# Kernel tuning notes

Hardware: AMD Instinct MI355X
Metric: run time of the kernel (lower is better)

The kernel has to match this reference:

```python
import jax, jax.numpy as jnp
import numpy as np

B = 131072
T = 30
H = 150
STATIC_D = 50


def _expm_sym2x2(S):
    """Closed-form V diag(exp(e)) V^T for symmetric (B,2,2) S.

    Equals exp(tr/2) * (cosh(d) I + sinh(d)/d * (S - tr/2 I)), d = sqrt(((a-c)/2)^2 + b^2).
    This is exactly what torch.symeig + exp(e) reconstruction computes.
    """
    a = S[:, 0, 0]
    b = S[:, 0, 1]
    c = S[:, 1, 1]
    half_tr = 0.5 * (a + c)
    half_diff = 0.5 * (a - c)
    disc = jnp.sqrt(half_diff * half_diff + b * b)
    d = jnp.maximum(disc, 1e-12)
    sinhc = jnp.sinh(d) / d
    coshd = jnp.cosh(disc)
    scale = jnp.exp(half_tr)
    m00 = scale * (coshd + sinhc * half_diff)
    m11 = scale * (coshd - sinhc * half_diff)
    m01 = scale * (sinhc * b)
    row0 = jnp.stack([m00, m01], axis=-1)
    row1 = jnp.stack([m01, m11], axis=-1)
    return jnp.stack([row0, row1], axis=-2)  # (B,2,2)


def setup_inputs() -> dict:
    key = jax.random.key(0)
    ks = jax.random.split(key, 12)
    s = lambda fan_in: 1.0 / np.sqrt(fan_in)
    inp = {
        "static": jax.random.normal(ks[0], (B, STATIC_D), jnp.float32),
        "init_velocity": jax.random.normal(ks[1], (B, 2), jnp.float32),
        "init_position": jax.random.normal(ks[2], (B, 2), jnp.float32),
        "z": jax.random.normal(ks[3], (T, B, 2), jnp.float32),
        # GRU params (PyTorch layout: gates [r, z, n] stacked along dim 0)
        "W_ih": jax.random.uniform(ks[4], (3 * H, T * 2), jnp.float32, -s(H), s(H)),
        "W_hh": jax.random.uniform(ks[5], (3 * H, H), jnp.float32, -s(H), s(H)),
        "b_ih": jax.random.uniform(ks[6], (3 * H,), jnp.float32, -s(H), s(H)),
        "b_hh": jax.random.uniform(ks[7], (3 * H,), jnp.float32, -s(H), s(H)),
        # MLP params
        "W1": jax.random.uniform(ks[8], (50, H + STATIC_D), jnp.float32, -s(H + STATIC_D), s(H + STATIC_D)),
        "b1": jax.random.uniform(ks[9], (50,), jnp.float32, -s(H + STATIC_D), s(H + STATIC_D)),
        "W2": jax.random.uniform(ks[10], (6, 50), jnp.float32, -s(50), s(50)),
        "b2": jax.random.uniform(ks[11], (6,), jnp.float32, -s(50), s(50)),
    }
    return inp


def reference(static, init_velocity, init_position, z, W_ih, W_hh, b_ih, b_hh, W1, b1, W2, b2):
    batch = static.shape[0]
    h0 = jnp.zeros((batch, H), jnp.float32)
    xbuf0 = jnp.zeros((batch, T, 2), jnp.float32)

    def step(carry, inp):
        h, xbuf, dx, x_prev = carry
        i, zi = inp
        x_flat = xbuf.reshape(batch, T * 2)
        # GRU cell (single layer, seq_len 1)
        gi = x_flat @ W_ih.T + b_ih
        gh = h @ W_hh.T + b_hh
        ir, iz, inn = jnp.split(gi, 3, axis=1)
        hr, hz, hn = jnp.split(gh, 3, axis=1)
        r = jax.nn.sigmoid(ir + hr)
        zg = jax.nn.sigmoid(iz + hz)
        n = jnp.tanh(inn + r * hn)
        h_new = (1.0 - zg) * n + zg * h
        # MLP on [dynamic_encoding, static]
        ds = jnp.concatenate([h_new, static], axis=1)
        o = jax.nn.softplus(ds @ W1.T + b1)
        o = jax.nn.softplus(o @ W2.T + b2)
        mu_hat = o[:, :2]
        sig_hat = o[:, 2:].reshape(batch, 2, 2)
        S = sig_hat + jnp.swapaxes(sig_hat, 1, 2)
        sigma = _expm_sym2x2(S)
        mu = x_prev + dx + mu_hat
        x_ = jnp.einsum('bij,bj->bi', sigma, zi) + mu
        xbuf = jax.lax.dynamic_update_slice(xbuf, x_[:, None, :], (0, i, 0))
        return (h_new, xbuf, x_ - x_prev, x_), (mu, sigma, x_)

    _, (mu, sigma, x) = jax.lax.scan(
        step, (h0, xbuf0, init_velocity, init_position), (jnp.arange(T), z)
    )
    return mu, sigma, x  # (30,B,2), (30,B,2,2), (30,B,2)
```

## Files before the change

### kernel.cpp

```cpp
#include <hip/hip_runtime.h>
#include <math.h>


typedef _Float16 f16;
typedef _Float16 f16x8 __attribute__((ext_vector_type(8)));
typedef float    f32x4 __attribute__((ext_vector_type(4)));

constexpr int BTOT = 131072;
constexpr int TSTEPS = 30;
constexpr int H  = 150;
constexpr int SD = 50;
constexpr int BT = 16;
constexpr int NT = 512;
constexpr int NBLK = 256;
constexpr int NGRP = BTOT / (NBLK * BT);

constexpr int HP = 160;
constexpr int NP = 480;
constexpr int AHS = 232;
constexpr int O1S = 72;

constexpr int WS_WIHT  = 0;
constexpr int WS_BFRAG = 115200;

constexpr int SIG_OFF = TSTEPS * BTOT * 2;
constexpr int X_OFF   = SIG_OFF + TSTEPS * BTOT * 4;

__device__ __forceinline__ float fexp(float x)  { return __builtin_amdgcn_exp2f(x * 1.44269504f); }
__device__ __forceinline__ float sigm(float x)  { return __builtin_amdgcn_rcpf(1.f + __builtin_amdgcn_exp2f(-1.44269504f * x)); }
__device__ __forceinline__ float tanh_(float x) { return fmaf(-2.f, __builtin_amdgcn_rcpf(1.f + __builtin_amdgcn_exp2f(2.88539008f * x)), 1.f); }
__device__ __forceinline__ float softplus_(float v) {
    float e = __builtin_amdgcn_exp2f(-1.44269504f * fabsf(v));
    return fmaxf(v, 0.f) + 0.69314718f * __builtin_amdgcn_logf(1.f + e);
}

__global__ void r2p2_prep(const float* __restrict__ Wih, float* __restrict__ ws) {
    int id = blockIdx.x * 256 + threadIdx.x;
    if (id >= TSTEPS * NP) return;
    int s = id / NP, tp = id - s * NP;
    int g = tp / HP, off = tp - g * HP;
    float2 v = make_float2(0.f, 0.f);
    if (off < H) {
        const float* row = Wih + (g * H + off) * (2 * TSTEPS);
        v.x = row[2 * s];
        v.y = row[2 * s + 1];
    }
    ((float2*)ws)[id] = v;
}

__global__ void r2p2_prep2(const float* __restrict__ Whh, f16* __restrict__ wsB) {
    int id = blockIdx.x * 256 + threadIdx.x;
    if (id >= 9600) return;
    int lane = id & 63, rest = id >> 6;
    int kk = rest % 5, kg = rest / 5;
    int g = kg % 3, k = kg / 3;
    int lr = lane & 15, lq = lane >> 4;
    int nr = k * 16 + lr;
    f16x8 v;
    #pragma unroll
    for (int j = 0; j < 8; ++j) {
        int cc = kk * 32 + lq * 8 + j;
        float x = (nr < H && cc < H) ? Whh[(g * H + nr) * H + cc] : 0.f;
        v[j] = (f16)x;
    }
    *(f16x8*)(wsB + (size_t)id * 8) = v;
}

__global__ __launch_bounds__(NT, 2) void r2p2_main(
    const float* __restrict__ statp, const float* __restrict__ initv,
    const float* __restrict__ initp, const float* __restrict__ zp,
    const float* __restrict__ bih,   const float* __restrict__ bhh,
    const float* __restrict__ W1,    const float* __restrict__ b1,
    const float* __restrict__ W2,    const float* __restrict__ b2,
    const float* __restrict__ wihT,  const f16* __restrict__ wsB,
    float* __restrict__ out)
{
    __shared__ __align__(16) f16   sA[BT * AHS];
    __shared__ __align__(16) f16   sW1[64 * AHS];
    __shared__ __align__(16) f16   sO1[16 * O1S];
    __shared__ __align__(16) f16   sW2[16 * O1S];
    __shared__ __align__(16) float sO2[16 * 8];
    __shared__ __align__(16) float sZ[TSTEPS * 32];
    __shared__ __align__(16) float sOUT[TSTEPS * 16 * 8];
    __shared__ __align__(16) float sXC[32];
    __shared__ __align__(16) float sXP[32];
    __shared__ __align__(16) float sDX[32];

    const int t  = threadIdx.x;
    const int w  = t >> 6;
    const int l  = t & 63;
    const int lr = l & 15;
    const int lq = l >> 4;

    int ntr = 0, tr0 = 0;
    if (w < 4)       { ntr = 1; tr0 = w; }
    else if (w >= 5) { ntr = 2; tr0 = 4 + (w - 5) * 2; }

    for (int i = t; i < BT * AHS / 2; i += NT) ((unsigned*)sA)[i] = 0u;
    for (int i = t; i < 64 * AHS; i += NT) {
        int r = i / AHS, k = i - r * AHS;
        float v = 0.f;
        if (r < SD && k < 224) {
            if (k < H) v = W1[r * 200 + k];
            else if (k >= HP && k < HP + SD) v = W1[r * 200 + H + (k - HP)];
        }
        sW1[i] = (f16)v;
    }
    for (int i = t; i < 16 * O1S; i += NT) {
        int r = i / O1S, k = i - r * O1S;
        sW2[i] = (f16)((r < 6 && k < SD) ? W2[r * SD + k] : 0.f);
        sO1[i] = (f16)0.f;
    }

    f16x8 bfrag[2][3][5];
    #pragma unroll
    for (int tt = 0; tt < 2; ++tt) {
        if (tt < ntr) {
            int k = tr0 + tt;
            #pragma unroll
            for (int g = 0; g < 3; ++g)
                #pragma unroll
                for (int kk = 0; kk < 5; ++kk)
                    bfrag[tt][g][kk] = *(const f16x8*)(wsB + ((size_t)((k * 3 + g) * 5 + kk) * 64 + l) * 8);
        }
    }
    float cR[2], cZ[2], cNi[2], cNh[2];
    #pragma unroll
    for (int tt = 0; tt < 2; ++tt) {
        cR[tt] = cZ[tt] = cNi[tt] = cNh[tt] = 0.f;
        if (tt < ntr) {
            int u = (tr0 + tt) * 16 + lr;
            if (u < H) {
                cR[tt]  = bih[u]         + bhh[u];
                cZ[tt]  = bih[H + u]     + bhh[H + u];
                cNi[tt] = bih[2 * H + u];
                cNh[tt] = bhh[2 * H + u];
            }
        }
    }
    const int   p3col  = w * 16 + lr;
    const float b1reg  = (w < 4 && p3col < SD) ? b1[p3col] : 0.f;
    const float b2reg  = (lr < 6) ? b2[lr] : 0.f;

    float hreg[2][4];
    f32x4 acc[2][3];
    f32x4 gi[2][3];
    float2 wvp[2][3];

    for (int grp = 0; grp < NGRP; ++grp) {
        const int bg0 = (grp * NBLK + blockIdx.x) * BT;
        __syncthreads();
        for (int i = t; i < BT * SD; i += NT) {
            int b = i / SD, k = i - b * SD;
            sA[b * AHS + HP + k] = (f16)statp[(bg0 + b) * SD + k];
        }
        for (int i = t; i < TSTEPS * 32; i += NT)
            sZ[i] = zp[((size_t)(i >> 5) * BTOT + bg0) * 2 + (i & 31)];
        if (t < 2 * BT) {
            sXP[t] = initp[bg0 * 2 + t];
            sDX[t] = initv[bg0 * 2 + t];
        }
        #pragma unroll
        for (int tt = 0; tt < 2; ++tt) {
            #pragma unroll
            for (int j = 0; j < 4; ++j) hreg[tt][j] = 0.f;
            #pragma unroll
            for (int g = 0; g < 3; ++g) acc[tt][g] = (f32x4){0.f, 0.f, 0.f, 0.f};
            gi[tt][0] = (f32x4){cR[tt],  cR[tt],  cR[tt],  cR[tt]};
            gi[tt][1] = (f32x4){cZ[tt],  cZ[tt],  cZ[tt],  cZ[tt]};
            gi[tt][2] = (f32x4){cNi[tt], cNi[tt], cNi[tt], cNi[tt]};
        }
        __syncthreads();

        for (int s = 0; s < TSTEPS; ++s) {
            if (ntr > 0) {
                if (s > 0) {
                    f32x4 xa = *(const f32x4*)&sXC[lq * 8];
                    f32x4 xb = *(const f32x4*)&sXC[lq * 8 + 4];
                    #pragma unroll
                    for (int tt = 0; tt < 2; ++tt) {
                        if (tt < ntr) {
                            #pragma unroll
                            for (int g = 0; g < 3; ++g) {
                                float2 wv = wvp[tt][g];
                                gi[tt][g][0] = fmaf(wv.x, xa[0], fmaf(wv.y, xa[1], gi[tt][g][0]));
                                gi[tt][g][1] = fmaf(wv.x, xa[2], fmaf(wv.y, xa[3], gi[tt][g][1]));
                                gi[tt][g][2] = fmaf(wv.x, xb[0], fmaf(wv.y, xb[1], gi[tt][g][2]));
                                gi[tt][g][3] = fmaf(wv.x, xb[2], fmaf(wv.y, xb[3], gi[tt][g][3]));
                            }
                        }
                    }
                }
                #pragma unroll
                for (int tt = 0; tt < 2; ++tt) {
                    if (tt < ntr) {
                        int u = (tr0 + tt) * 16 + lr;
                        #pragma unroll
                        for (int j = 0; j < 4; ++j) {
                            float r  = sigm(acc[tt][0][j] + gi[tt][0][j]);
                            float zg = sigm(acc[tt][1][j] + gi[tt][1][j]);
                            float n  = tanh_(gi[tt][2][j] + r * (acc[tt][2][j] + cNh[tt]));
                            float hv = (1.f - zg) * n + zg * hreg[tt][j];
                            hreg[tt][j] = hv;
                            if (u < H) sA[(lq * 4 + j) * AHS + u] = (f16)hv;
                        }
                    }
                }
            }
            __syncthreads();

            if (ntr > 0 && s + 1 < TSTEPS) {
                const float* wT = wihT + (size_t)s * (NP * 2);
                #pragma unroll
                for (int tt = 0; tt < 2; ++tt) {
                    if (tt < ntr) {
                        int u = (tr0 + tt) * 16 + lr;
                        #pragma unroll
                        for (int g = 0; g < 3; ++g)
                            wvp[tt][g] = *(const float2*)(wT + (g * HP + u) * 2);
                    }
                }
            }

            if (w < 4) {
                f32x4 a3 = (f32x4){0.f, 0.f, 0.f, 0.f};
                #pragma unroll
                for (int kk = 0; kk < 7; ++kk) {
                    f16x8 av = *(const f16x8*)(sA  + lr    * AHS + kk * 32 + lq * 8);
                    f16x8 bv = *(const f16x8*)(sW1 + p3col * AHS + kk * 32 + lq * 8);
                    a3 = __builtin_amdgcn_mfma_f32_16x16x32_f16(av, bv, a3, 0, 0, 0);
                }
                if (p3col < SD) {
                    #pragma unroll
                    for (int j = 0; j < 4; ++j)
                        sO1[(lq * 4 + j) * O1S + p3col] = (f16)softplus_(a3[j] + b1reg);
                }
            } else if (w >= 5 && s + 1 < TSTEPS) {
                f16x8 af[5];
                #pragma unroll
                for (int kk = 0; kk < 5; ++kk)
                    af[kk] = *(const f16x8*)(sA + lr * AHS + kk * 32 + lq * 8);
                #pragma unroll
                for (int tt = 0; tt < 2; ++tt) {
                    #pragma unroll
                    for (int g = 0; g < 3; ++g) {
                        acc[tt][g] = (f32x4){0.f, 0.f, 0.f, 0.f};
                        #pragma unroll
                        for (int kk = 0; kk < 5; ++kk)
                            acc[tt][g] = __builtin_amdgcn_mfma_f32_16x16x32_f16(af[kk], bfrag[tt][g][kk], acc[tt][g], 0, 0, 0);
                    }
                }
            }
            __syncthreads();

            if (w == 4) {
                f32x4 a4 = (f32x4){0.f, 0.f, 0.f, 0.f};
                #pragma unroll
                for (int kk = 0; kk < 2; ++kk) {
                    f16x8 av = *(const f16x8*)(sO1 + lr * O1S + kk * 32 + lq * 8);
                    f16x8 bv = *(const f16x8*)(sW2 + lr * O1S + kk * 32 + lq * 8);
                    a4 = __builtin_amdgcn_mfma_f32_16x16x32_f16(av, bv, a4, 0, 0, 0);
                }
                if (lr < 6) {
                    #pragma unroll
                    for (int j = 0; j < 4; ++j)
                        sO2[(lq * 4 + j) * 8 + lr] = softplus_(a4[j] + b2reg);
                }
                asm volatile("s_waitcnt lgkmcnt(0)" ::: "memory");
                if (l < BT) {
                    const int b = l;
                    f32x4  v0 = *(const f32x4*)&sO2[b * 8];
                    float2 v1 = *(const float2*)&sO2[b * 8 + 4];
                    float mh0 = v0[0], mh1 = v0[1];
                    float a = 2.f * v0[2], bb2 = v0[3] + v1.x, c = 2.f * v1.y;
                    float htr = 0.5f * (a + c), hdf = 0.5f * (a - c);
                    float disc = sqrtf(hdf * hdf + bb2 * bb2);
                    float d = fmaxf(disc, 1e-12f);
                    float ep = fexp(d), em = fexp(-d);
                    float sinhc = (0.5f * (ep - em)) * __builtin_amdgcn_rcpf(d);
                    float coshd = 0.5f * (ep + em);
                    float scale = fexp(htr);
                    float m00 = scale * (coshd + sinhc * hdf);
                    float m11 = scale * (coshd - sinhc * hdf);
                    float m01 = scale * (sinhc * bb2);

                    float z0 = sZ[s * 32 + 2 * b], z1 = sZ[s * 32 + 2 * b + 1];
                    float xp0 = sXP[2 * b], xp1 = sXP[2 * b + 1];
                    float mu0 = xp0 + sDX[2 * b]     + mh0;
                    float mu1 = xp1 + sDX[2 * b + 1] + mh1;
                    float x0 = fmaf(m00, z0, fmaf(m01, z1, mu0));
                    float x1 = fmaf(m01, z0, fmaf(m11, z1, mu1));

                    float* st = &sOUT[(s * 16 + b) * 8];
                    *(float4*)(st)     = make_float4(mu0, mu1, m00, m01);
                    *(float4*)(st + 4) = make_float4(m11, x0, x1, 0.f);

                    sXC[2 * b] = x0;       sXC[2 * b + 1] = x1;
                    sDX[2 * b] = x0 - xp0; sDX[2 * b + 1] = x1 - xp1;
                    sXP[2 * b] = x0;       sXP[2 * b + 1] = x1;
                }
            } else if (w < 4 && s + 1 < TSTEPS) {
                f16x8 af[5];
                #pragma unroll
                for (int kk = 0; kk < 5; ++kk)
                    af[kk] = *(const f16x8*)(sA + lr * AHS + kk * 32 + lq * 8);
                #pragma unroll
                for (int g = 0; g < 3; ++g) {
                    acc[0][g] = (f32x4){0.f, 0.f, 0.f, 0.f};
                    #pragma unroll
                    for (int kk = 0; kk < 5; ++kk)
                        acc[0][g] = __builtin_amdgcn_mfma_f32_16x16x32_f16(af[kk], bfrag[0][g][kk], acc[0][g], 0, 0, 0);
                }
            }
            __syncthreads();
        }

        if (t < TSTEPS * 16) {
            int s = t >> 4, b = t & 15;
            const float* src = &sOUT[(s * 16 + b) * 8];
            const size_t oi = (size_t)s * BTOT + bg0 + b;
            *(float2*)(out + oi * 2)           = make_float2(src[0], src[1]);
            *(float4*)(out + SIG_OFF + oi * 4) = make_float4(src[2], src[3], src[3], src[4]);
            *(float2*)(out + X_OFF + oi * 2)   = make_float2(src[5], src[6]);
        }
    }
}

extern "C" void kernel_launch(void* const* d_in, const int* in_sizes, int n_in,
                              void* d_out, int out_size, void* d_ws, size_t ws_size,
                              hipStream_t stream) {
    const float* statp = (const float*)d_in[0];
    const float* initv = (const float*)d_in[1];
    const float* initp = (const float*)d_in[2];
    const float* zp    = (const float*)d_in[3];
    const float* Wih   = (const float*)d_in[4];
    const float* Whh   = (const float*)d_in[5];
    const float* bih   = (const float*)d_in[6];
    const float* bhh   = (const float*)d_in[7];
    const float* W1    = (const float*)d_in[8];
    const float* b1    = (const float*)d_in[9];
    const float* W2    = (const float*)d_in[10];
    const float* b2    = (const float*)d_in[11];
    float* out  = (float*)d_out;
    float* wihT = (float*)((char*)d_ws + WS_WIHT);
    f16*   wsB  = (f16*)  ((char*)d_ws + WS_BFRAG);

    r2p2_prep <<<(TSTEPS * NP + 255) / 256, 256, 0, stream>>>(Wih, wihT);
    r2p2_prep2<<<(9600 + 255) / 256, 256, 0, stream>>>(Whh, wsB);
    r2p2_main<<<NBLK, NT, 0, stream>>>(
        statp, initv, initp, zp, bih, bhh, W1, b1, W2, b2, wihT, wsB, out);
}
```

Measured before the change: 2.191 ms.

## Double block to 16 waves, one GRU tile per wave, dedicated MLP waves

After: 3.032 ms. 1.38x slower.

```diff
diff --git a/kernel.cpp b/kernel.cpp
--- a/kernel.cpp
+++ b/kernel.cpp
@@ -11,7 +11,7 @@
 constexpr int H  = 150;
 constexpr int SD = 50;
 constexpr int BT = 16;
-constexpr int NT = 512;
+constexpr int NT = 1024;
 constexpr int NBLK = 256;
 constexpr int NGRP = BTOT / (NBLK * BT);
 
@@ -66,7 +66,7 @@
     *(f16x8*)(wsB + (size_t)id * 8) = v;
 }
 
-__global__ __launch_bounds__(NT, 2) void r2p2_main(
+__global__ __launch_bounds__(NT, 4) void r2p2_main(
     const float* __restrict__ statp, const float* __restrict__ initv,
     const float* __restrict__ initp, const float* __restrict__ zp,
     const float* __restrict__ bih,   const float* __restrict__ bhh,
@@ -92,9 +92,11 @@
     const int lr = l & 15;
     const int lq = l >> 4;
 
-    int ntr = 0, tr0 = 0;
-    if (w < 4)       { ntr = 1; tr0 = w; }
-    else if (w >= 5) { ntr = 2; tr0 = 4 + (w - 5) * 2; }
+    const bool owner = (w < 10);
+    const bool mlp1w = (w >= 10 && w < 14);
+    const bool mlp2w = (w == 14);
+    const int  trip  = w;
+    const int  uu    = trip * 16 + lr;
 
     for (int i = t; i < BT * AHS / 2; i += NT) ((unsigned*)sA)[i] = 0u;
     for (int i = t; i < 64 * AHS; i += NT) {
@@ -112,40 +114,29 @@
         sO1[i] = (f16)0.f;
     }
 
-    f16x8 bfrag[2][3][5];
-    #pragma unroll
-    for (int tt = 0; tt < 2; ++tt) {
-        if (tt < ntr) {
-            int k = tr0 + tt;
+    f16x8 bfrag[3][5];
+    if (owner) {
+        #pragma unroll
+        for (int g = 0; g < 3; ++g)
             #pragma unroll
-            for (int g = 0; g < 3; ++g)
-                #pragma unroll
-                for (int kk = 0; kk < 5; ++kk)
-                    bfrag[tt][g][kk] = *(const f16x8*)(wsB + ((size_t)((k * 3 + g) * 5 + kk) * 64 + l) * 8);
-        }
-    }
-    float cR[2], cZ[2], cNi[2], cNh[2];
-    #pragma unroll
-    for (int tt = 0; tt < 2; ++tt) {
-        cR[tt] = cZ[tt] = cNi[tt] = cNh[tt] = 0.f;
-        if (tt < ntr) {
-            int u = (tr0 + tt) * 16 + lr;
-            if (u < H) {
-                cR[tt]  = bih[u]         + bhh[u];
-                cZ[tt]  = bih[H + u]     + bhh[H + u];
-                cNi[tt] = bih[2 * H + u];
-                cNh[tt] = bhh[2 * H + u];
-            }
-        }
-    }
-    const int   p3col  = w * 16 + lr;
-    const float b1reg  = (w < 4 && p3col < SD) ? b1[p3col] : 0.f;
-    const float b2reg  = (lr < 6) ? b2[lr] : 0.f;
-
-    float hreg[2][4];
-    f32x4 acc[2][3];
-    f32x4 gi[2][3];
-    float2 wvp[2][3];
+            for (int kk = 0; kk < 5; ++kk)
+                bfrag[g][kk] = *(const f16x8*)(wsB + ((size_t)((trip * 3 + g) * 5 + kk) * 64 + l) * 8);
+    }
+    float cR = 0.f, cZ = 0.f, cNi = 0.f, cNh = 0.f;
+    if (owner && uu < H) {
+        cR  = bih[uu]         + bhh[uu];
+        cZ  = bih[H + uu]     + bhh[H + uu];
+        cNi = bih[2 * H + uu];
+        cNh = bhh[2 * H + uu];
+    }
+    const int   p3col = (w - 10) * 16 + lr;
+    const float b1reg = (mlp1w && p3col < SD) ? b1[p3col] : 0.f;
+    const float b2reg = (mlp2w && lr < 6) ? b2[lr] : 0.f;
+
+    float  hreg[4];
+    f32x4  acc[3];
+    f32x4  gi[3];
+    float2 wvp[3];
 
     for (int grp = 0; grp < NGRP; ++grp) {
         const int bg0 = (grp * NBLK + blockIdx.x) * BT;
@@ -160,69 +151,51 @@
             sXP[t] = initp[bg0 * 2 + t];
             sDX[t] = initv[bg0 * 2 + t];
         }
-        #pragma unroll
-        for (int tt = 0; tt < 2; ++tt) {
+        if (owner) {
             #pragma unroll
-            for (int j = 0; j < 4; ++j) hreg[tt][j] = 0.f;
+            for (int j = 0; j < 4; ++j) hreg[j] = 0.f;
             #pragma unroll
-            for (int g = 0; g < 3; ++g) acc[tt][g] = (f32x4){0.f, 0.f, 0.f, 0.f};
-            gi[tt][0] = (f32x4){cR[tt],  cR[tt],  cR[tt],  cR[tt]};
-            gi[tt][1] = (f32x4){cZ[tt],  cZ[tt],  cZ[tt],  cZ[tt]};
-            gi[tt][2] = (f32x4){cNi[tt], cNi[tt], cNi[tt], cNi[tt]};
+            for (int g = 0; g < 3; ++g) acc[g] = (f32x4){0.f, 0.f, 0.f, 0.f};
+            gi[0] = (f32x4){cR,  cR,  cR,  cR};
+            gi[1] = (f32x4){cZ,  cZ,  cZ,  cZ};
+            gi[2] = (f32x4){cNi, cNi, cNi, cNi};
         }
         __syncthreads();
 
         for (int s = 0; s < TSTEPS; ++s) {
-            if (ntr > 0) {
+            if (owner) {
                 if (s > 0) {
                     f32x4 xa = *(const f32x4*)&sXC[lq * 8];
                     f32x4 xb = *(const f32x4*)&sXC[lq * 8 + 4];
                     #pragma unroll
-                    for (int tt = 0; tt < 2; ++tt) {
-                        if (tt < ntr) {
-                            #pragma unroll
-                            for (int g = 0; g < 3; ++g) {
-                                float2 wv = wvp[tt][g];
-                                gi[tt][g][0] = fmaf(wv.x, xa[0], fmaf(wv.y, xa[1], gi[tt][g][0]));
-                                gi[tt][g][1] = fmaf(wv.x, xa[2], fmaf(wv.y, xa[3], gi[tt][g][1]));
-                                gi[tt][g][2] = fmaf(wv.x, xb[0], fmaf(wv.y, xb[1], gi[tt][g][2]));
-                                gi[tt][g][3] = fmaf(wv.x, xb[2], fmaf(wv.y, xb[3], gi[tt][g][3]));
-                            }
-                        }
+                    for (int g = 0; g < 3; ++g) {
+                        float2 wv = wvp[g];
+                        gi[g][0] = fmaf(wv.x, xa[0], fmaf(wv.y, xa[1], gi[g][0]));
+                        gi[g][1] = fmaf(wv.x, xa[2], fmaf(wv.y, xa[3], gi[g][1]));
+                        gi[g][2] = fmaf(wv.x, xb[0], fmaf(wv.y, xb[1], gi[g][2]));
+                        gi[g][3] = fmaf(wv.x, xb[2], fmaf(wv.y, xb[3], gi[g][3]));
                     }
                 }
                 #pragma unroll
-                for (int tt = 0; tt < 2; ++tt) {
-                    if (tt < ntr) {
-                        int u = (tr0 + tt) * 16 + lr;
-                        #pragma unroll
-                        for (int j = 0; j < 4; ++j) {
-                            float r  = sigm(acc[tt][0][j] + gi[tt][0][j]);
-                            float zg = sigm(acc[tt][1][j] + gi[tt][1][j]);
-                            float n  = tanh_(gi[tt][2][j] + r * (acc[tt][2][j] + cNh[tt]));
-                            float hv = (1.f - zg) * n + zg * hreg[tt][j];
-                            hreg[tt][j] = hv;
-                            if (u < H) sA[(lq * 4 + j) * AHS + u] = (f16)hv;
-                        }
-                    }
+                for (int j = 0; j < 4; ++j) {
+                    float r  = sigm(acc[0][j] + gi[0][j]);
+                    float zg = sigm(acc[1][j] + gi[1][j]);
+                    float n  = tanh_(gi[2][j] + r * (acc[2][j] + cNh));
+                    float hv = (1.f - zg) * n + zg * hreg[j];
+                    hreg[j] = hv;
+                    if (uu < H) sA[(lq * 4 + j) * AHS + uu] = (f16)hv;
                 }
             }
             __syncthreads();
 
-            if (ntr > 0 && s + 1 < TSTEPS) {
+            if (owner && s + 1 < TSTEPS) {
                 const float* wT = wihT + (size_t)s * (NP * 2);
                 #pragma unroll
-                for (int tt = 0; tt < 2; ++tt) {
-                    if (tt < ntr) {
-                        int u = (tr0 + tt) * 16 + lr;
-                        #pragma unroll
-                        for (int g = 0; g < 3; ++g)
-                            wvp[tt][g] = *(const float2*)(wT + (g * HP + u) * 2);
-                    }
-                }
+                for (int g = 0; g < 3; ++g)
+                    wvp[g] = *(const float2*)(wT + (g * HP + uu) * 2);
             }
 
-            if (w < 4) {
+            if (mlp1w) {
                 f32x4 a3 = (f32x4){0.f, 0.f, 0.f, 0.f};
                 #pragma unroll
                 for (int kk = 0; kk < 7; ++kk) {
@@ -235,25 +208,22 @@
                     for (int j = 0; j < 4; ++j)
                         sO1[(lq * 4 + j) * O1S + p3col] = (f16)softplus_(a3[j] + b1reg);
                 }
-            } else if (w >= 5 && s + 1 < TSTEPS) {
+            } else if (owner && s + 1 < TSTEPS) {
                 f16x8 af[5];
                 #pragma unroll
                 for (int kk = 0; kk < 5; ++kk)
                     af[kk] = *(const f16x8*)(sA + lr * AHS + kk * 32 + lq * 8);
                 #pragma unroll
-                for (int tt = 0; tt < 2; ++tt) {
+                for (int g = 0; g < 3; ++g) {
+                    acc[g] = (f32x4){0.f, 0.f, 0.f, 0.f};
                     #pragma unroll
-                    for (int g = 0; g < 3; ++g) {
-                        acc[tt][g] = (f32x4){0.f, 0.f, 0.f, 0.f};
-                        #pragma unroll
-                        for (int kk = 0; kk < 5; ++kk)
-                            acc[tt][g] = __builtin_amdgcn_mfma_f32_16x16x32_f16(af[kk], bfrag[tt][g][kk], acc[tt][g], 0, 0, 0);
-                    }
+                    for (int kk = 0; kk < 5; ++kk)
+                        acc[g] = __builtin_amdgcn_mfma_f32_16x16x32_f16(af[kk], bfrag[g][kk], acc[g], 0, 0, 0);
                 }
             }
             __syncthreads();
 
-            if (w == 4) {
+            if (mlp2w) {
                 f32x4 a4 = (f32x4){0.f, 0.f, 0.f, 0.f};
                 #pragma unroll
                 for (int kk = 0; kk < 2; ++kk) {
@@ -298,18 +268,6 @@
                     sXC[2 * b] = x0;       sXC[2 * b + 1] = x1;
                     sDX[2 * b] = x0 - xp0; sDX[2 * b + 1] = x1 - xp1;
                     sXP[2 * b] = x0;       sXP[2 * b + 1] = x1;
-                }
-            } else if (w < 4 && s + 1 < TSTEPS) {
-                f16x8 af[5];
-                #pragma unroll
-                for (int kk = 0; kk < 5; ++kk)
-                    af[kk] = *(const f16x8*)(sA + lr * AHS + kk * 32 + lq * 8);
-                #pragma unroll
-                for (int g = 0; g < 3; ++g) {
-                    acc[0][g] = (f32x4){0.f, 0.f, 0.f, 0.f};
-                    #pragma unroll
-                    for (int kk = 0; kk < 5; ++kk)
-                        acc[0][g] = __builtin_amdgcn_mfma_f32_16x16x32_f16(af[kk], bfrag[0][g][kk], acc[0][g], 0, 0, 0);
                 }
             }
             __syncthreads();
```
